# Performance work log

Hardware: AMD Instinct MI355X
Metric: run time of the kernel (lower is better)

The kernel has to match this reference:

```python
import jax, jax.numpy as jnp
import numpy as np

def _round_ste(x):
    # StraightThrough: forward = round, backward = identity
    return x + jax.lax.stop_gradient(jnp.round(x) - x)

def setup_inputs() -> dict:
    key = jax.random.key(0)
    k1, k2, k3, k4, k5 = jax.random.split(key, 5)
    in_f, out_f, n_tok = 4096, 4096, 8192
    return {
        "input": jax.random.normal(k1, (n_tok, in_f), dtype=jnp.float32),
        "weight": jax.random.normal(k2, (out_f, in_f), dtype=jnp.float32),
        "bias": jax.random.normal(k3, (out_f,), dtype=jnp.float32),
        "w_scale": jax.random.uniform(k4, (1,), dtype=jnp.float32),
        "b_scale": jax.random.uniform(k5, (1,), dtype=jnp.float32),
    }

def reference(input, weight, bias, w_scale, b_scale):
    # straight-through rounding of quantized latents (use_straight_through=True, compress_bias=True)
    w_q = _round_ste(weight)
    b_q = _round_ste(bias)
    # decoder: per-tensor affine dequantization
    w_dec = w_scale * w_q          # [out, in]
    b_dec = b_scale * b_q          # [out]
    # F.linear: input @ weight.T + bias
    return jnp.einsum('ni,oi->no', input, w_dec) + b_dec
```

## Files before the change

### kernel.cpp

```cpp
#include <hip/hip_runtime.h>
#include <stdint.h>


using bf16x8  = __attribute__((ext_vector_type(8))) __bf16;
using floatx4 = __attribute__((ext_vector_type(4))) float;
using ushort8 = __attribute__((ext_vector_type(8))) unsigned short;

__device__ __forceinline__ unsigned short f2bf_rne(float x) {
    unsigned int u = __float_as_uint(x);
    return (unsigned short)((u + 0x7fffu + ((u >> 16) & 1u)) >> 16);
}

__device__ __forceinline__ void load_lds16(const unsigned short* g, unsigned short* l) {
    __builtin_amdgcn_global_load_lds(
        (__attribute__((address_space(1))) void*)g,
        (__attribute__((address_space(3))) void*)l,
        16, 0, 0);
}

template <bool ROUND>
__global__ __launch_bounds__(256) void cvt_bf16(const float* __restrict__ in,
                                                unsigned short* __restrict__ out) {
    const long long i = ((long long)blockIdx.x * 256 + threadIdx.x) * 8;
    float4 v0 = *(const float4*)(in + i);
    float4 v1 = *(const float4*)(in + i + 4);
    float f[8] = {v0.x, v0.y, v0.z, v0.w, v1.x, v1.y, v1.z, v1.w};
    ushort8 o;
#pragma unroll
    for (int j = 0; j < 8; ++j) {
        float x = ROUND ? rintf(f[j]) : f[j];
        o[j] = f2bf_rne(x);
    }
    *(ushort8*)(out + i) = o;
}

__global__ __launch_bounds__(256) void gemm_bf16_bt(
    const unsigned short* __restrict__ A,
    const unsigned short* __restrict__ B,
    const float* __restrict__ bias,
    const float* __restrict__ wscale_p,
    const float* __restrict__ bscale_p,
    float* __restrict__ C,
    int M, int N, int K) {
    constexpr int BM = 128, BN = 128, BK = 32;
    __shared__ unsigned short ldsA[BM * BK];
    __shared__ unsigned short ldsB[BN * BK];

    const int tid  = threadIdx.x;
    const int wave = tid >> 6;
    const int lane = tid & 63;
    const int quad = lane >> 4;
    const int l16  = lane & 15;

    const int bm = blockIdx.y * BM;
    const int bn = blockIdx.x * BN;
    const int wm = (wave >> 1) * 64;
    const int wn = (wave & 1) * 64;

    const float wsc = wscale_p[0];
    const float bsc = bscale_p[0];

    float badd[4];
#pragma unroll
    for (int ni = 0; ni < 4; ++ni)
        badd[ni] = bsc * rintf(bias[bn + wn + ni * 16 + l16]);

    const int c0 = wave * 128 + lane;
    const int c1 = c0 + 64;
    const int r0 = c0 >> 2, k0 = (c0 & 3) * 8;
    const int r1 = c1 >> 2, k1 = (c1 & 3) * 8;
    const unsigned short* gA0 = A + (size_t)(bm + r0) * K + k0;
    const unsigned short* gA1 = A + (size_t)(bm + r1) * K + k1;
    const unsigned short* gB0 = B + (size_t)(bn + r0) * K + k0;
    const unsigned short* gB1 = B + (size_t)(bn + r1) * K + k1;
    unsigned short* lA0 = &ldsA[(wave * 128 + 0) * 8];
    unsigned short* lA1 = &ldsA[(wave * 128 + 64) * 8];
    unsigned short* lB0 = &ldsB[(wave * 128 + 0) * 8];
    unsigned short* lB1 = &ldsB[(wave * 128 + 64) * 8];

    floatx4 acc[4][4] = {};

    for (int kt = 0; kt < K; kt += BK) {
        load_lds16(gA0 + kt, lA0);
        load_lds16(gA1 + kt, lA1);
        load_lds16(gB0 + kt, lB0);
        load_lds16(gB1 + kt, lB1);
        __syncthreads();

        bf16x8 af[4], bfr[4];
#pragma unroll
        for (int mi = 0; mi < 4; ++mi) {
            const int off = (wm + mi * 16 + l16) * BK + quad * 8;
            af[mi] = __builtin_bit_cast(bf16x8, *(const ushort8*)&ldsA[off]);
        }
#pragma unroll
        for (int ni = 0; ni < 4; ++ni) {
            const int off = (wn + ni * 16 + l16) * BK + quad * 8;
            bfr[ni] = __builtin_bit_cast(bf16x8, *(const ushort8*)&ldsB[off]);
        }
#pragma unroll
        for (int mi = 0; mi < 4; ++mi)
#pragma unroll
            for (int ni = 0; ni < 4; ++ni)
                acc[mi][ni] = __builtin_amdgcn_mfma_f32_16x16x32_bf16(
                    af[mi], bfr[ni], acc[mi][ni], 0, 0, 0);
        __syncthreads();
    }

#pragma unroll
    for (int mi = 0; mi < 4; ++mi) {
        const int m0 = bm + wm + mi * 16 + quad * 4;
#pragma unroll
        for (int ni = 0; ni < 4; ++ni) {
            const int n = bn + wn + ni * 16 + l16;
#pragma unroll
            for (int r = 0; r < 4; ++r)
                C[(size_t)(m0 + r) * N + n] = acc[mi][ni][r] * wsc + badd[ni];
        }
    }
}

__global__ __launch_bounds__(256) void fallback_gemm(
    const float* __restrict__ A, const float* __restrict__ W,
    const float* __restrict__ bias, const float* __restrict__ wsp,
    const float* __restrict__ bsp, float* __restrict__ C, int M, int N, int K) {
    const int n = blockIdx.x * 256 + threadIdx.x;
    const int m = blockIdx.y;
    if (n >= N || m >= M) return;
    float s = 0.f;
    for (int k = 0; k < K; ++k)
        s += A[(size_t)m * K + k] * rintf(W[(size_t)n * K + k]);
    C[(size_t)m * N + n] = s * wsp[0] + bsp[0] * rintf(bias[n]);
}

extern "C" void kernel_launch(void* const* d_in, const int* in_sizes, int n_in,
                              void* d_out, int out_size, void* d_ws, size_t ws_size,
                              hipStream_t stream) {
    const float* input  = (const float*)d_in[0];
    const float* weight = (const float*)d_in[1];
    const float* bias   = (const float*)d_in[2];
    const float* wscale = (const float*)d_in[3];
    const float* bscale = (const float*)d_in[4];
    float* out = (float*)d_out;

    const int N = in_sizes[2];
    const int K = in_sizes[1] / N;
    const int M = in_sizes[0] / K;

    const size_t needA = (size_t)M * K * sizeof(unsigned short);
    const size_t needB = (size_t)N * K * sizeof(unsigned short);

    if (ws_size >= needA + needB && (M % 128) == 0 && (N % 128) == 0 &&
        (K % 32) == 0 && ((size_t)M * K % 2048) == 0 && ((size_t)N * K % 2048) == 0) {
        unsigned short* Abf = (unsigned short*)d_ws;
        unsigned short* Bbf = (unsigned short*)((char*)d_ws + needA);
        cvt_bf16<false><<<(unsigned)((size_t)M * K / 2048), 256, 0, stream>>>(input, Abf);
        cvt_bf16<true ><<<(unsigned)((size_t)N * K / 2048), 256, 0, stream>>>(weight, Bbf);
        dim3 grid(N / 128, M / 128);
        gemm_bf16_bt<<<grid, 256, 0, stream>>>(Abf, Bbf, bias, wscale, bscale, out, M, N, K);
    } else {
        dim3 grid((N + 255) / 256, M);
        fallback_gemm<<<grid, 256, 0, stream>>>(input, weight, bias, wscale, bscale, out, M, N, K);
    }
}
```

Measured before the change: 602.7 us.

## Merge bf16 conversion kernels and XOR-swizzle LDS tiles to avoid bank conflicts

The two fp32-to-bf16 conversion launches become one kernel that handles input and weight with 4-wide vectors, saving one launch. In the GEMM, the mapping from global loads to LDS is changed so each row's 8-element k-chunk lands at an XOR-swizzled slot, and the fragment reads apply the matching swizzle. This is meant to cut LDS bank conflicts on the 16-byte fragment reads. The conversion now does narrower per-thread work, which could reduce its memory throughput a little.

```diff
diff --git a/kernel.cpp b/kernel.cpp
--- a/kernel.cpp
+++ b/kernel.cpp
@@ -4,7 +4,8 @@
 
 using bf16x8  = __attribute__((ext_vector_type(8))) __bf16;
 using floatx4 = __attribute__((ext_vector_type(4))) float;
-using ushort8 = __attribute__((ext_vector_type(8))) unsigned short;
+using us8     = __attribute__((ext_vector_type(8))) unsigned short;
+using us4     = __attribute__((ext_vector_type(4))) unsigned short;
 
 __device__ __forceinline__ unsigned short f2bf_rne(float x) {
     unsigned int u = __float_as_uint(x);
@@ -18,20 +19,23 @@
         16, 0, 0);
 }
 
-template <bool ROUND>
-__global__ __launch_bounds__(256) void cvt_bf16(const float* __restrict__ in,
-                                                unsigned short* __restrict__ out) {
-    const long long i = ((long long)blockIdx.x * 256 + threadIdx.x) * 8;
-    float4 v0 = *(const float4*)(in + i);
-    float4 v1 = *(const float4*)(in + i + 4);
-    float f[8] = {v0.x, v0.y, v0.z, v0.w, v1.x, v1.y, v1.z, v1.w};
-    ushort8 o;
-#pragma unroll
-    for (int j = 0; j < 8; ++j) {
-        float x = ROUND ? rintf(f[j]) : f[j];
-        o[j] = f2bf_rne(x);
+__global__ __launch_bounds__(256) void cvt_both(
+    const float* __restrict__ inA, unsigned short* __restrict__ outA, long long nA4,
+    const float* __restrict__ inB, unsigned short* __restrict__ outB, long long nB4) {
+    const long long i = (long long)blockIdx.x * 256 + threadIdx.x;
+    if (i < nA4) {
+        float4 v = ((const float4*)inA)[i];
+        us4 o = { f2bf_rne(v.x), f2bf_rne(v.y), f2bf_rne(v.z), f2bf_rne(v.w) };
+        ((us4*)outA)[i] = o;
+    } else {
+        const long long j = i - nA4;
+        if (j < nB4) {
+            float4 v = ((const float4*)inB)[j];
+            us4 o = { f2bf_rne(rintf(v.x)), f2bf_rne(rintf(v.y)),
+                      f2bf_rne(rintf(v.z)), f2bf_rne(rintf(v.w)) };
+            ((us4*)outB)[j] = o;
+        }
     }
-    *(ushort8*)(out + i) = o;
 }
 
 __global__ __launch_bounds__(256) void gemm_bf16_bt(
@@ -42,9 +46,9 @@
     const float* __restrict__ bscale_p,
     float* __restrict__ C,
     int M, int N, int K) {
-    constexpr int BM = 128, BN = 128, BK = 32;
+    constexpr int BM = 128, BK = 32;
     __shared__ unsigned short ldsA[BM * BK];
-    __shared__ unsigned short ldsB[BN * BK];
+    __shared__ unsigned short ldsB[BM * BK];
 
     const int tid  = threadIdx.x;
     const int wave = tid >> 6;
@@ -53,7 +57,7 @@
     const int l16  = lane & 15;
 
     const int bm = blockIdx.y * BM;
-    const int bn = blockIdx.x * BN;
+    const int bn = blockIdx.x * BM;
     const int wm = (wave >> 1) * 64;
     const int wn = (wave & 1) * 64;
 
@@ -65,18 +69,19 @@
     for (int ni = 0; ni < 4; ++ni)
         badd[ni] = bsc * rintf(bias[bn + wn + ni * 16 + l16]);
 
-    const int c0 = wave * 128 + lane;
-    const int c1 = c0 + 64;
-    const int r0 = c0 >> 2, k0 = (c0 & 3) * 8;
-    const int r1 = c1 >> 2, k1 = (c1 & 3) * 8;
-    const unsigned short* gA0 = A + (size_t)(bm + r0) * K + k0;
-    const unsigned short* gA1 = A + (size_t)(bm + r1) * K + k1;
-    const unsigned short* gB0 = B + (size_t)(bn + r0) * K + k0;
-    const unsigned short* gB1 = B + (size_t)(bn + r1) * K + k1;
+    const int r0 = wave * 32 + (lane >> 2);
+    const int kc = ((lane & 3) ^ ((lane >> 3) & 3)) * 8;
+    const unsigned short* gA0 = A + (size_t)(bm + r0) * K + kc;
+    const unsigned short* gA1 = A + (size_t)(bm + r0 + 16) * K + kc;
+    const unsigned short* gB0 = B + (size_t)(bn + r0) * K + kc;
+    const unsigned short* gB1 = B + (size_t)(bn + r0 + 16) * K + kc;
     unsigned short* lA0 = &ldsA[(wave * 128 + 0) * 8];
     unsigned short* lA1 = &ldsA[(wave * 128 + 64) * 8];
     unsigned short* lB0 = &ldsB[(wave * 128 + 0) * 8];
     unsigned short* lB1 = &ldsB[(wave * 128 + 64) * 8];
+
+    const int xr = (l16 >> 1) & 3;
+    const int sa = (quad ^ xr) * 8;
 
     floatx4 acc[4][4] = {};
 
@@ -90,13 +95,13 @@
         bf16x8 af[4], bfr[4];
 #pragma unroll
         for (int mi = 0; mi < 4; ++mi) {
-            const int off = (wm + mi * 16 + l16) * BK + quad * 8;
-            af[mi] = __builtin_bit_cast(bf16x8, *(const ushort8*)&ldsA[off]);
+            const int off = (wm + mi * 16 + l16) * BK + sa;
+            af[mi] = __builtin_bit_cast(bf16x8, *(const us8*)&ldsA[off]);
         }
 #pragma unroll
         for (int ni = 0; ni < 4; ++ni) {
-            const int off = (wn + ni * 16 + l16) * BK + quad * 8;
-            bfr[ni] = __builtin_bit_cast(bf16x8, *(const ushort8*)&ldsB[off]);
+            const int off = (wn + ni * 16 + l16) * BK + sa;
+            bfr[ni] = __builtin_bit_cast(bf16x8, *(const us8*)&ldsB[off]);
         }
 #pragma unroll
         for (int mi = 0; mi < 4; ++mi)
@@ -151,11 +156,14 @@
     const size_t needB = (size_t)N * K * sizeof(unsigned short);
 
     if (ws_size >= needA + needB && (M % 128) == 0 && (N % 128) == 0 &&
-        (K % 32) == 0 && ((size_t)M * K % 2048) == 0 && ((size_t)N * K % 2048) == 0) {
+        (K % 32) == 0) {
         unsigned short* Abf = (unsigned short*)d_ws;
         unsigned short* Bbf = (unsigned short*)((char*)d_ws + needA);
-        cvt_bf16<false><<<(unsigned)((size_t)M * K / 2048), 256, 0, stream>>>(input, Abf);
-        cvt_bf16<true ><<<(unsigned)((size_t)N * K / 2048), 256, 0, stream>>>(weight, Bbf);
+        const long long nA4 = (long long)M * K / 4;
+        const long long nB4 = (long long)N * K / 4;
+        const long long nthr = nA4 + nB4;
+        cvt_both<<<(unsigned)((nthr + 255) / 256), 256, 0, stream>>>(
+            input, Abf, nA4, weight, Bbf, nB4);
         dim3 grid(N / 128, M / 128);
         gemm_bf16_bt<<<grid, 256, 0, stream>>>(Abf, Bbf, bias, wscale, bscale, out, M, N, K);
     } else {
```

Measured after the change: 594.6 us. About the same (-1.3%).
